# Optimization experiments

Hardware: AMD Instinct MI355X
Metric: run time of the kernel (lower is better)

## Reference

```python
import jax, jax.numpy as jnp
import numpy as np

N = 1_000_000   # total nodes
H = 128         # hidden_dim
B = 16_384      # num graphs in batch


def setup_inputs() -> dict:
    key = jax.random.key(0)
    k0, k1, k2, k3 = jax.random.split(key, 4)
    x = jax.random.normal(k0, (N, H), dtype=jnp.float32)
    batch_index = jnp.sort(jax.random.randint(k1, (N,), 0, B))
    s = 1.0 / np.sqrt(H)
    W1 = jax.random.normal(k2, (H, H), dtype=jnp.float32) * s
    b1 = jnp.zeros((H,), dtype=jnp.float32)
    W2 = jax.random.normal(k3, (H, 1), dtype=jnp.float32) * s
    b2 = jnp.zeros((1,), dtype=jnp.float32)
    return {"x": x, "W1": W1, "b1": b1, "W2": W2, "b2": b2,
            "batch_index": batch_index, "num_graphs": B}


def reference(x, W1, b1, W2, b2, batch_index, num_graphs):
    # --- global mean pool ---
    seg_sum = jax.ops.segment_sum(x, batch_index, num_segments=num_graphs)
    counts = jax.ops.segment_sum(jnp.ones((x.shape[0],), x.dtype), batch_index,
                                 num_segments=num_graphs)
    mean = seg_sum / jnp.maximum(counts, 1.0)[:, None]          # [B, H]
    # --- global max pool ---
    mx = jax.ops.segment_max(x, batch_index, num_segments=num_graphs)  # [B, H]
    # --- attentional aggregation: gate MLP -> segment softmax -> weighted sum ---
    h = jax.nn.silu(x @ W1 + b1)                                # [N, H]
    gate = (h @ W2 + b2)[:, 0]                                  # [N]
    gmax = jax.ops.segment_max(gate, batch_index, num_segments=num_graphs)
    e = jnp.exp(gate - gmax[batch_index])
    denom = jax.ops.segment_sum(e, batch_index, num_segments=num_graphs)
    att = e / denom[batch_index]                                # [N] per-segment softmax
    attn_out = jax.ops.segment_sum(att[:, None] * x, batch_index,
                                   num_segments=num_graphs)     # [B, H]
    return jnp.concatenate([mean, mx, attn_out], axis=-1)       # [B, 3H]
```

## Files before the change

### kernel.cpp

```cpp
#include <hip/hip_runtime.h>
#include <hip/hip_bf16.h>
#include <math.h>

#define H 128
#define TILE_M 64
#define LDS_STRIDE 136

typedef __attribute__((ext_vector_type(8))) short bf16x8;
typedef __attribute__((ext_vector_type(4))) float f32x4;

__device__ __forceinline__ short f2bf(float f) {
  union { float f; unsigned u; } v; v.f = f;
  unsigned r = v.u + 0x7fffu + ((v.u >> 16) & 1u);
  return (short)(r >> 16);
}

__global__ void prep_kernel(const float* __restrict__ w1, short* __restrict__ w1t) {
  int i = blockIdx.x * blockDim.x + threadIdx.x;
  if (i >= H * H) return;
  int k = i >> 7, n = i & (H - 1);
  w1t[n * H + k] = f2bf(w1[k * H + n]);
}

__global__ void bounds_kernel(const int* __restrict__ bi, int* __restrict__ seg_start,
                              int N, int B) {
  int n = blockIdx.x * blockDim.x + threadIdx.x;
  if (n >= N) return;
  int cur = bi[n];
  int prev = (n == 0) ? -1 : bi[n - 1];
  for (int g = prev + 1; g <= cur; ++g) seg_start[g] = n;
  if (n == N - 1) {
    for (int g = cur + 1; g <= B; ++g) seg_start[g] = N;
  }
}

__global__ __launch_bounds__(256) void gate_kernel(
    const float* __restrict__ x, const short* __restrict__ w1t,
    const float* __restrict__ b1, const float* __restrict__ w2,
    const float* __restrict__ b2, float* __restrict__ gate, int N)
{
  __shared__ __align__(16) short xs[TILE_M * LDS_STRIDE];
  __shared__ float gate_lds[TILE_M];

  const int tid = threadIdx.x;
  const int base = blockIdx.x * TILE_M;

  if (tid < TILE_M) gate_lds[tid] = 0.0f;

  {
    const int colg = (tid & 31) * 4;
    const int row0 = tid >> 5;
#pragma unroll
    for (int i = 0; i < 8; ++i) {
      int row = row0 + 8 * i;
      int gr = base + row;
      float4 v = make_float4(0.f, 0.f, 0.f, 0.f);
      if (gr < N) v = *(const float4*)(x + (size_t)gr * H + colg);
      short4 s = make_short4(f2bf(v.x), f2bf(v.y), f2bf(v.z), f2bf(v.w));
      *(short4*)(&xs[row * LDS_STRIDE + colg]) = s;
    }
  }
  __syncthreads();

  const int w = tid >> 6;
  const int lane = tid & 63;
  const int l15 = lane & 15;
  const int q = lane >> 4;

  f32x4 acc[4][2] = {};
#pragma unroll
  for (int kc = 0; kc < H; kc += 32) {
    bf16x8 a[4], b[2];
#pragma unroll
    for (int mt = 0; mt < 4; ++mt) {
      a[mt] = *(const bf16x8*)(&xs[(16 * mt + l15) * LDS_STRIDE + kc + 8 * q]);
    }
#pragma unroll
    for (int nt = 0; nt < 2; ++nt) {
      int n = 32 * w + 16 * nt + l15;
      b[nt] = *(const bf16x8*)(w1t + n * H + kc + 8 * q);
    }
#pragma unroll
    for (int mt = 0; mt < 4; ++mt)
#pragma unroll
      for (int nt = 0; nt < 2; ++nt)
        acc[mt][nt] = __builtin_amdgcn_mfma_f32_16x16x32_bf16(a[mt], b[nt], acc[mt][nt], 0, 0, 0);
  }

  const int c0 = 32 * w + l15;
  const int c1 = c0 + 16;
  const float w2c0 = w2[c0], w2c1 = w2[c1];
  const float b1c0 = b1[c0], b1c1 = b1[c1];
#pragma unroll
  for (int mt = 0; mt < 4; ++mt) {
#pragma unroll
    for (int r = 0; r < 4; ++r) {
      float h0 = acc[mt][0][r] + b1c0;
      float h1 = acc[mt][1][r] + b1c1;
      float s0 = h0 / (1.0f + __expf(-h0));
      float s1 = h1 / (1.0f + __expf(-h1));
      float p = s0 * w2c0 + s1 * w2c1;
      p += __shfl_xor(p, 1);
      p += __shfl_xor(p, 2);
      p += __shfl_xor(p, 4);
      p += __shfl_xor(p, 8);
      if (l15 == 0) atomicAdd(&gate_lds[16 * mt + 4 * q + r], p);
    }
  }
  __syncthreads();
  if (tid < TILE_M) {
    int gr = base + tid;
    if (gr < N) gate[gr] = gate_lds[tid] + b2[0];
  }
}

__global__ __launch_bounds__(128) void pool_kernel(
    const float* __restrict__ x, const float* __restrict__ gate,
    const int* __restrict__ seg_start, float* __restrict__ out)
{
  const int g = blockIdx.x;
  const int h = threadIdx.x;
  const int s = seg_start[g];
  const int e = seg_start[g + 1];

  float sum = 0.f, mx = -INFINITY;
  float accv = 0.f, m_run = -INFINITY, l_run = 0.f;

  for (int n = s; n < e; ++n) {
    float xv = x[(size_t)n * H + h];
    float gt = gate[n];
    sum += xv;
    mx = fmaxf(mx, xv);
    float m_new = fmaxf(m_run, gt);
    float corr = __expf(m_run - m_new);
    float ev = __expf(gt - m_new);
    l_run = l_run * corr + ev;
    accv = accv * corr + ev * xv;
    m_run = m_new;
  }

  const int cnt = e - s;
  float* og = out + (size_t)g * (3 * H);
  og[h] = sum / fmaxf((float)cnt, 1.0f);
  og[H + h] = mx;
  og[2 * H + h] = (cnt > 0) ? (accv / l_run) : 0.0f;
}

extern "C" void kernel_launch(void* const* d_in, const int* in_sizes, int n_in,
                              void* d_out, int out_size, void* d_ws, size_t ws_size,
                              hipStream_t stream)
{
  const float* x   = (const float*)d_in[0];
  const float* w1  = (const float*)d_in[1];
  const float* b1  = (const float*)d_in[2];
  const float* w2  = (const float*)d_in[3];
  const float* b2  = (const float*)d_in[4];
  const int*  bidx = (const int*)d_in[5];

  const int N  = in_sizes[5];
  const int Bn = out_size / (3 * H);

  char* ws = (char*)d_ws;
  size_t off = 0;
  float* gate = (float*)(ws + off);
  off += (size_t)N * sizeof(float);
  off = (off + 255) & ~(size_t)255;
  int* seg_start = (int*)(ws + off);
  off += (size_t)(Bn + 1) * sizeof(int);
  off = (off + 255) & ~(size_t)255;
  short* w1t = (short*)(ws + off);

  prep_kernel<<<(H * H + 255) / 256, 256, 0, stream>>>(w1, w1t);
  bounds_kernel<<<(N + 255) / 256, 256, 0, stream>>>(bidx, seg_start, N, Bn);
  gate_kernel<<<(N + TILE_M - 1) / TILE_M, 256, 0, stream>>>(x, w1t, b1, w2, b2, gate, N);
  pool_kernel<<<Bn, H, 0, stream>>>(x, gate, seg_start, (float*)d_out);
}
```

Baseline: 890.7 us.

## Fuse gate MLP and segment pooling into one per-graph kernel

After: 885.6 us. Within noise of the previous version (-0.6%).

```diff
diff --git a/kernel.cpp b/kernel.cpp
--- a/kernel.cpp
+++ b/kernel.cpp
@@ -3,8 +3,8 @@
 #include <math.h>
 
 #define H 128
-#define TILE_M 64
-#define LDS_STRIDE 136
+#define TILE 64
+#define XB_STRIDE 136
 
 typedef __attribute__((ext_vector_type(8))) short bf16x8;
 typedef __attribute__((ext_vector_type(4))) float f32x4;
@@ -34,116 +34,133 @@
   }
 }
 
-__global__ __launch_bounds__(256) void gate_kernel(
+__global__ __launch_bounds__(256) void fused_kernel(
     const float* __restrict__ x, const short* __restrict__ w1t,
     const float* __restrict__ b1, const float* __restrict__ w2,
-    const float* __restrict__ b2, float* __restrict__ gate, int N)
+    const float* __restrict__ b2, const int* __restrict__ seg_start,
+    float* __restrict__ out)
 {
-  __shared__ __align__(16) short xs[TILE_M * LDS_STRIDE];
-  __shared__ float gate_lds[TILE_M];
+  __shared__ __align__(16) float xf[TILE][H];
+  __shared__ __align__(16) short xb[TILE * XB_STRIDE];
+  __shared__ float gate_lds[TILE];
+  __shared__ float merge_lds[5][H];
 
-  const int tid = threadIdx.x;
-  const int base = blockIdx.x * TILE_M;
+  const int g = blockIdx.x;
+  const int s = seg_start[g];
+  const int e = seg_start[g + 1];
+  const int R = e - s;
 
-  if (tid < TILE_M) gate_lds[tid] = 0.0f;
+  const int tid  = threadIdx.x;
+  const int w    = tid >> 6;
+  const int lane = tid & 63;
+  const int l15  = lane & 15;
+  const int q    = lane >> 4;
 
-  {
-    const int colg = (tid & 31) * 4;
-    const int row0 = tid >> 5;
+  const int h    = tid & (H - 1);
+  const int half = tid >> 7;
+  float sum = 0.f, mx = -INFINITY;
+  float m_run = -INFINITY, l_run = 0.f, accv = 0.f;
+
+  const float b2v  = b2[0];
+  const int   c0   = 32 * w + l15, c1 = c0 + 16;
+  const float w2c0 = w2[c0], w2c1 = w2[c1];
+  const float b1c0 = b1[c0], b1c1 = b1[c1];
+
+  for (int t0 = 0; t0 < R; t0 += TILE) {
+    const int Rt = min(TILE, R - t0);
+
+    {
+      const int colg = (tid & 31) * 4;
+      const int row0 = tid >> 5;
 #pragma unroll
-    for (int i = 0; i < 8; ++i) {
-      int row = row0 + 8 * i;
-      int gr = base + row;
-      float4 v = make_float4(0.f, 0.f, 0.f, 0.f);
-      if (gr < N) v = *(const float4*)(x + (size_t)gr * H + colg);
-      short4 s = make_short4(f2bf(v.x), f2bf(v.y), f2bf(v.z), f2bf(v.w));
-      *(short4*)(&xs[row * LDS_STRIDE + colg]) = s;
+      for (int i = 0; i < 8; ++i) {
+        int row = row0 + 8 * i;
+        float4 v = make_float4(0.f, 0.f, 0.f, 0.f);
+        if (row < Rt) v = *(const float4*)(x + (size_t)(s + t0 + row) * H + colg);
+        *(float4*)(&xf[row][colg]) = v;
+        short4 sv = make_short4(f2bf(v.x), f2bf(v.y), f2bf(v.z), f2bf(v.w));
+        *(short4*)(&xb[row * XB_STRIDE + colg]) = sv;
+      }
     }
+    if (tid < TILE) gate_lds[tid] = 0.0f;
+    __syncthreads();
+
+    f32x4 acc[4][2] = {};
+#pragma unroll
+    for (int kc = 0; kc < H; kc += 32) {
+      bf16x8 a[4], b[2];
+#pragma unroll
+      for (int mt = 0; mt < 4; ++mt)
+        a[mt] = *(const bf16x8*)(&xb[(16 * mt + l15) * XB_STRIDE + kc + 8 * q]);
+#pragma unroll
+      for (int nt = 0; nt < 2; ++nt) {
+        int n = 32 * w + 16 * nt + l15;
+        b[nt] = *(const bf16x8*)(w1t + n * H + kc + 8 * q);
+      }
+#pragma unroll
+      for (int mt = 0; mt < 4; ++mt)
+#pragma unroll
+        for (int nt = 0; nt < 2; ++nt)
+          acc[mt][nt] = __builtin_amdgcn_mfma_f32_16x16x32_bf16(a[mt], b[nt], acc[mt][nt], 0, 0, 0);
+    }
+
+#pragma unroll
+    for (int mt = 0; mt < 4; ++mt) {
+#pragma unroll
+      for (int r = 0; r < 4; ++r) {
+        float h0 = acc[mt][0][r] + b1c0;
+        float h1 = acc[mt][1][r] + b1c1;
+        float s0 = h0 / (1.0f + __expf(-h0));
+        float s1 = h1 / (1.0f + __expf(-h1));
+        float p = s0 * w2c0 + s1 * w2c1;
+        p += __shfl_xor(p, 1);
+        p += __shfl_xor(p, 2);
+        p += __shfl_xor(p, 4);
+        p += __shfl_xor(p, 8);
+        if (l15 == 0) atomicAdd(&gate_lds[16 * mt + 4 * q + r], p);
+      }
+    }
+    __syncthreads();
+
+    for (int r = half; r < Rt; r += 2) {
+      float gt = gate_lds[r] + b2v;
+      float xv = xf[r][h];
+      sum += xv;
+      mx = fmaxf(mx, xv);
+      float m_new = fmaxf(m_run, gt);
+      float corr = __expf(m_run - m_new);
+      float ev   = __expf(gt - m_new);
+      l_run = l_run * corr + ev;
+      accv  = accv * corr + ev * xv;
+      m_run = m_new;
+    }
+    __syncthreads();
+  }
+
+  if (half == 1) {
+    merge_lds[0][h] = sum;
+    merge_lds[1][h] = mx;
+    merge_lds[2][h] = m_run;
+    merge_lds[3][h] = l_run;
+    merge_lds[4][h] = accv;
   }
   __syncthreads();
+  if (half == 0) {
+    float sum2 = merge_lds[0][h], mx2 = merge_lds[1][h];
+    float m2 = merge_lds[2][h], l2 = merge_lds[3][h], a2 = merge_lds[4][h];
+    sum += sum2;
+    mx = fmaxf(mx, mx2);
+    float m_new = fmaxf(m_run, m2);
+    float cA = __expf(m_run - m_new);
+    float cB = __expf(m2 - m_new);
+    l_run = l_run * cA + l2 * cB;
+    accv  = accv * cA + a2 * cB;
 
-  const int w = tid >> 6;
-  const int lane = tid & 63;
-  const int l15 = lane & 15;
-  const int q = lane >> 4;
-
-  f32x4 acc[4][2] = {};
-#pragma unroll
-  for (int kc = 0; kc < H; kc += 32) {
-    bf16x8 a[4], b[2];
-#pragma unroll
-    for (int mt = 0; mt < 4; ++mt) {
-      a[mt] = *(const bf16x8*)(&xs[(16 * mt + l15) * LDS_STRIDE + kc + 8 * q]);
-    }
-#pragma unroll
-    for (int nt = 0; nt < 2; ++nt) {
-      int n = 32 * w + 16 * nt + l15;
-      b[nt] = *(const bf16x8*)(w1t + n * H + kc + 8 * q);
-    }
-#pragma unroll
-    for (int mt = 0; mt < 4; ++mt)
-#pragma unroll
-      for (int nt = 0; nt < 2; ++nt)
-        acc[mt][nt] = __builtin_amdgcn_mfma_f32_16x16x32_bf16(a[mt], b[nt], acc[mt][nt], 0, 0, 0);
+    float* og = out + (size_t)g * (3 * H);
+    og[h]         = sum / fmaxf((float)R, 1.0f);
+    og[H + h]     = mx;
+    og[2 * H + h] = (R > 0) ? (accv / l_run) : 0.0f;
   }
-
-  const int c0 = 32 * w + l15;
-  const int c1 = c0 + 16;
-  const float w2c0 = w2[c0], w2c1 = w2[c1];
-  const float b1c0 = b1[c0], b1c1 = b1[c1];
-#pragma unroll
-  for (int mt = 0; mt < 4; ++mt) {
-#pragma unroll
-    for (int r = 0; r < 4; ++r) {
-      float h0 = acc[mt][0][r] + b1c0;
-      float h1 = acc[mt][1][r] + b1c1;
-      float s0 = h0 / (1.0f + __expf(-h0));
-      float s1 = h1 / (1.0f + __expf(-h1));
-      float p = s0 * w2c0 + s1 * w2c1;
-      p += __shfl_xor(p, 1);
-      p += __shfl_xor(p, 2);
-      p += __shfl_xor(p, 4);
-      p += __shfl_xor(p, 8);
-      if (l15 == 0) atomicAdd(&gate_lds[16 * mt + 4 * q + r], p);
-    }
-  }
-  __syncthreads();
-  if (tid < TILE_M) {
-    int gr = base + tid;
-    if (gr < N) gate[gr] = gate_lds[tid] + b2[0];
-  }
-}
-
-__global__ __launch_bounds__(128) void pool_kernel(
-    const float* __restrict__ x, const float* __restrict__ gate,
-    const int* __restrict__ seg_start, float* __restrict__ out)
-{
-  const int g = blockIdx.x;
-  const int h = threadIdx.x;
-  const int s = seg_start[g];
-  const int e = seg_start[g + 1];
-
-  float sum = 0.f, mx = -INFINITY;
-  float accv = 0.f, m_run = -INFINITY, l_run = 0.f;
-
-  for (int n = s; n < e; ++n) {
-    float xv = x[(size_t)n * H + h];
-    float gt = gate[n];
-    sum += xv;
-    mx = fmaxf(mx, xv);
-    float m_new = fmaxf(m_run, gt);
-    float corr = __expf(m_run - m_new);
-    float ev = __expf(gt - m_new);
-    l_run = l_run * corr + ev;
-    accv = accv * corr + ev * xv;
-    m_run = m_new;
-  }
-
-  const int cnt = e - s;
-  float* og = out + (size_t)g * (3 * H);
-  og[h] = sum / fmaxf((float)cnt, 1.0f);
-  og[H + h] = mx;
-  og[2 * H + h] = (cnt > 0) ? (accv / l_run) : 0.0f;
 }
 
 extern "C" void kernel_launch(void* const* d_in, const int* in_sizes, int n_in,
@@ -162,9 +179,6 @@
 
   char* ws = (char*)d_ws;
   size_t off = 0;
-  float* gate = (float*)(ws + off);
-  off += (size_t)N * sizeof(float);
-  off = (off + 255) & ~(size_t)255;
   int* seg_start = (int*)(ws + off);
   off += (size_t)(Bn + 1) * sizeof(int);
   off = (off + 255) & ~(size_t)255;
@@ -172,6 +186,5 @@
 
   prep_kernel<<<(H * H + 255) / 256, 256, 0, stream>>>(w1, w1t);
   bounds_kernel<<<(N + 255) / 256, 256, 0, stream>>>(bidx, seg_start, N, Bn);
-  gate_kernel<<<(N + TILE_M - 1) / TILE_M, 256, 0, stream>>>(x, w1t, b1, w2, b2, gate, N);
-  pool_kernel<<<Bn, H, 0, stream>>>(x, gate, seg_start, (float*)d_out);
+  fused_kernel<<<Bn, 256, 0, stream>>>(x, w1t, b1, w2, b2, seg_start, (float*)d_out);
 }
```
